# Kernel tuning notes

Hardware: AMD Instinct MI355X
Metric: run time of the kernel (lower is better)

Reference implementation:

```python
import jax, jax.numpy as jnp
import numpy as np

N, E, H, ATOM, BOND, G, DEPTH = 100000, 400000, 256, 133, 14, 512, 4


def _lin(k, out_dim, in_dim):
    kw, kb = jax.random.split(k)
    s = 1.0 / np.sqrt(in_dim)
    w = jax.random.uniform(kw, (out_dim, in_dim), jnp.float32, -s, s)
    b = jax.random.uniform(kb, (out_dim,), jnp.float32, -s, s)
    return w, b


def setup_inputs() -> dict:
    key = jax.random.key(0)
    ks = jax.random.split(key, 16)
    # paired directed edges: edge 2i and 2i+1 are reverses of each other
    src_half = jax.random.randint(ks[0], (E // 2,), 0, N)
    dst_half = jax.random.randint(ks[1], (E // 2,), 0, N)
    edge_src = jnp.stack([src_half, dst_half], axis=1).reshape(-1)
    edge_dst = jnp.stack([dst_half, src_half], axis=1).reshape(-1)
    b2rev = jnp.arange(E, dtype=jnp.int64) ^ 1
    node_to_graph = jnp.sort(jax.random.randint(ks[2], (N,), 0, G))
    atom_feats = jax.random.normal(ks[3], (N, ATOM), jnp.float32)
    edge_feats = jax.random.normal(ks[4], (E, BOND), jnp.float32)
    edge_weights = jax.random.uniform(ks[5], (E,), jnp.float32)
    Wi, _ = _lin(ks[6], H, ATOM + BOND)  # W_initial, bias=False
    Wm_w, Wm_b = _lin(ks[7], H, H)
    Wn_w, Wn_b = _lin(ks[8], H, ATOM + H)
    nh0_w, nh0_b = _lin(ks[9], H, H)
    nh2_w, nh2_b = _lin(ks[10], ATOM, H)
    eh0_w, eh0_b = _lin(ks[11], H, H)
    eh2_w, eh2_b = _lin(ks[12], BOND, H)
    gh0_w, gh0_b = _lin(ks[13], H, H)
    gh2_w, gh2_b = _lin(ks[14], 1, H)
    return dict(atom_feats=atom_feats, edge_feats=edge_feats, edge_weights=edge_weights,
                Wi=Wi, Wm_w=Wm_w, Wm_b=Wm_b, Wn_w=Wn_w, Wn_b=Wn_b,
                nh0_w=nh0_w, nh0_b=nh0_b, nh2_w=nh2_w, nh2_b=nh2_b,
                eh0_w=eh0_w, eh0_b=eh0_b, eh2_w=eh2_w, eh2_b=eh2_b,
                gh0_w=gh0_w, gh0_b=gh0_b, gh2_w=gh2_w, gh2_b=gh2_b,
                edge_src=edge_src, edge_dst=edge_dst, b2rev=b2rev,
                node_to_graph=node_to_graph, depth=DEPTH, num_graphs=G)


def reference(atom_feats, edge_feats, edge_weights, Wi, Wm_w, Wm_b, Wn_w, Wn_b,
              nh0_w, nh0_b, nh2_w, nh2_b, eh0_w, eh0_b, eh2_w, eh2_b,
              gh0_w, gh0_b, gh2_w, gh2_b,
              edge_src, edge_dst, b2rev, node_to_graph, depth, num_graphs):
    Nn = atom_feats.shape[0]
    valid = b2rev >= 0
    rev_idx = jnp.where(valid, b2rev, 0)
    # initial edge hidden states: [E, H]
    h = jax.nn.relu(jnp.concatenate([atom_feats[edge_src], edge_feats], axis=1) @ Wi.T)
    for _ in range(depth):
        # weighted scatter-add of edge messages onto destination nodes: [N, H]
        M = jax.ops.segment_sum(edge_weights[:, None] * h, edge_dst, num_segments=Nn)
        rev_h = jnp.where(valid[:, None], h[rev_idx], 0.0)
        rev_w = jnp.where(valid, edge_weights[rev_idx], 0.0)
        msg = M[edge_src] - rev_w[:, None] * rev_h  # [E, H]
        h = jax.nn.relu(msg @ Wm_w.T + Wm_b)
    node_agg = jax.ops.segment_sum(edge_weights[:, None] * h, edge_dst, num_segments=Nn)
    node_repr = jax.nn.relu(jnp.concatenate([atom_feats, node_agg], axis=1) @ Wn_w.T + Wn_b)
    graph_embeds = jax.ops.segment_sum(node_repr, node_to_graph, num_segments=num_graphs)
    pred_node = jax.nn.relu(node_repr @ nh0_w.T + nh0_b) @ nh2_w.T + nh2_b
    pred_edge = jax.nn.relu(h @ eh0_w.T + eh0_b) @ eh2_w.T + eh2_b
    pred_graph = (jax.nn.relu(graph_embeds @ gh0_w.T + gh0_b) @ gh2_w.T + gh2_b).squeeze(-1)
    return (pred_node, pred_edge, pred_graph, graph_embeds, node_repr, h)
```

## Files before the change

kernel.cpp:

```cpp
#include <hip/hip_runtime.h>
#include <hip/hip_bf16.h>

#define HDIM 256
#define ATOMF 133
#define BONDF 14
#define DEPTH_HC 4
#define SCAN_CHUNK 1024
#define KWN 448

typedef short bf16x8 __attribute__((ext_vector_type(8)));
typedef float f32x4 __attribute__((ext_vector_type(4)));
typedef unsigned short u16x8 __attribute__((ext_vector_type(8)));
typedef unsigned short u16x4 __attribute__((ext_vector_type(4)));

__device__ inline float bf2f(unsigned short u) {
    unsigned int x = ((unsigned int)u) << 16;
    float f; __builtin_memcpy(&f, &x, 4); return f;
}
__device__ inline unsigned short f2bf(float f) {
    __hip_bfloat16 h = __float2bfloat16(f);
    unsigned short u; __builtin_memcpy(&u, &h, 2); return u;
}

__device__ inline void gload_lds16(const unsigned short* g, unsigned short* lds) {
    __builtin_amdgcn_global_load_lds(
        (const __attribute__((address_space(1))) unsigned int*)g,
        (__attribute__((address_space(3))) unsigned int*)lds, 16, 0, 0);
}

__global__ __launch_bounds__(512) void mfma_gemm_cat(
    const float* __restrict__ atom, const float* __restrict__ bond,
    const int* __restrict__ src, int E,
    const unsigned short* __restrict__ W,
    unsigned short* __restrict__ Cb)
{
    __shared__ unsigned short As[128 * 32];
    __shared__ unsigned short Bs[256 * 32];
    const int t = threadIdx.x;
    const int w = t >> 6, l = t & 63;
    const int m0 = blockIdx.x * 128;
    const int wr = w >> 2, wc = w & 3;

    f32x4 acc[4][4] = {};

    const int ar = t >> 2;
    const int ac0 = (t & 3) * 8;
    long long e_row = m0 + ar; if (e_row > E - 1) e_row = E - 1;
    const int sn = src[e_row];
    const float* arow = atom + (size_t)sn * ATOMF;
    const float* brow = bond + (size_t)e_row * BONDF;

    const int kcol = (l & 3) * 8;
    const int rowL = (w << 4) + (l >> 2);

    #pragma unroll
    for (int k0 = 0; k0 < 160; k0 += 32) {
        u16x8 o;
        const int c = k0 + ac0;
        if (k0 < 128) {
            #pragma unroll
            for (int i = 0; i < 8; ++i) o[i] = f2bf(arow[c + i]);
        } else {
            #pragma unroll
            for (int i = 0; i < 8; ++i) {
                int k = c + i;
                float v = 0.0f;
                if (k < ATOMF)              v = arow[k];
                else if (k < ATOMF + BONDF) v = brow[k - ATOMF];
                o[i] = f2bf(v);
            }
        }
        *(u16x8*)&As[ar * 32 + ac0] = o;
        gload_lds16(W + (size_t)rowL * 160 + k0 + kcol, Bs + (size_t)w * 512);
        gload_lds16(W + (size_t)(128 + rowL) * 160 + k0 + kcol, Bs + 4096 + (size_t)w * 512);
        __syncthreads();

        const int kq = (l >> 4) * 8;
        const int rbase = (wr << 6) + (l & 15);
        const int cbase = (wc << 6) + (l & 15);
        bf16x8 af[4], bfr[4];
        #pragma unroll
        for (int i = 0; i < 4; ++i) {
            af[i]  = *(const bf16x8*)&As[(rbase + i * 16) * 32 + kq];
            bfr[i] = *(const bf16x8*)&Bs[(cbase + i * 16) * 32 + kq];
        }
        #pragma unroll
        for (int mi = 0; mi < 4; ++mi)
            #pragma unroll
            for (int ni = 0; ni < 4; ++ni)
                acc[mi][ni] = __builtin_amdgcn_mfma_f32_16x16x32_bf16(
                    af[mi], bfr[ni], acc[mi][ni], 0, 0, 0);
        __syncthreads();
    }

    const int ccol = l & 15, crow = (l >> 4) * 4;
    #pragma unroll
    for (int ni = 0; ni < 4; ++ni) {
        int gn = (wc << 6) + ni * 16 + ccol;
        #pragma unroll
        for (int mi = 0; mi < 4; ++mi) {
            #pragma unroll
            for (int j = 0; j < 4; ++j) {
                long long gm = m0 + (wr << 6) + mi * 16 + crow + j;
                if (gm >= E) continue;
                float v = fmaxf(acc[mi][ni][j], 0.0f);
                Cb[(size_t)gm * HDIM + gn] = f2bf(v);
            }
        }
    }
}

__global__ __launch_bounds__(512) void mfma_gemm_msg(
    const unsigned short* __restrict__ Mb,
    const unsigned short* __restrict__ h,
    const float* __restrict__ w,
    const int* __restrict__ src, int E,
    const unsigned short* __restrict__ W,
    const float* __restrict__ bias,
    float* __restrict__ Cf,
    unsigned short* __restrict__ Cb)
{
    __shared__ unsigned short As[128 * 32];
    __shared__ unsigned short Bs[256 * 32];
    const int t = threadIdx.x;
    const int wv = t >> 6, l = t & 63;
    const int m0 = blockIdx.x * 128;
    const int wr = wv >> 2, wc = wv & 3;

    f32x4 acc[4][4] = {};

    const int ar = t >> 2;
    const int ac0 = (t & 3) * 8;
    long long e_row = m0 + ar; if (e_row > E - 1) e_row = E - 1;
    const long long er1 = e_row ^ 1;
    const int sn = src[e_row];
    const float we1 = w[er1];

    const int kcol = (l & 3) * 8;
    const int rowL = (wv << 4) + (l >> 2);

    #pragma unroll
    for (int k0 = 0; k0 < 256; k0 += 32) {
        u16x8 Mv = *(const u16x8*)&Mb[(size_t)sn * HDIM + k0 + ac0];
        u16x8 hv = *(const u16x8*)&h[(size_t)er1 * HDIM + k0 + ac0];
        u16x8 o;
        #pragma unroll
        for (int i = 0; i < 8; ++i)
            o[i] = f2bf(bf2f(Mv[i]) - we1 * bf2f(hv[i]));
        *(u16x8*)&As[ar * 32 + ac0] = o;
        gload_lds16(W + (size_t)rowL * 256 + k0 + kcol, Bs + (size_t)wv * 512);
        gload_lds16(W + (size_t)(128 + rowL) * 256 + k0 + kcol, Bs + 4096 + (size_t)wv * 512);
        __syncthreads();

        const int kq = (l >> 4) * 8;
        const int rbase = (wr << 6) + (l & 15);
        const int cbase = (wc << 6) + (l & 15);
        bf16x8 af[4], bfr[4];
        #pragma unroll
        for (int i = 0; i < 4; ++i) {
            af[i]  = *(const bf16x8*)&As[(rbase + i * 16) * 32 + kq];
            bfr[i] = *(const bf16x8*)&Bs[(cbase + i * 16) * 32 + kq];
        }
        #pragma unroll
        for (int mi = 0; mi < 4; ++mi)
            #pragma unroll
            for (int ni = 0; ni < 4; ++ni)
                acc[mi][ni] = __builtin_amdgcn_mfma_f32_16x16x32_bf16(
                    af[mi], bfr[ni], acc[mi][ni], 0, 0, 0);
        __syncthreads();
    }

    const int ccol = l & 15, crow = (l >> 4) * 4;
    #pragma unroll
    for (int ni = 0; ni < 4; ++ni) {
        int gn = (wc << 6) + ni * 16 + ccol;
        float bv = bias[gn];
        #pragma unroll
        for (int mi = 0; mi < 4; ++mi) {
            #pragma unroll
            for (int j = 0; j < 4; ++j) {
                long long gm = m0 + (wr << 6) + mi * 16 + crow + j;
                if (gm >= E) continue;
                float v = fmaxf(acc[mi][ni][j] + bv, 0.0f);
                if (Cf) Cf[(size_t)gm * HDIM + gn] = v;
                Cb[(size_t)gm * HDIM + gn] = f2bf(v);
            }
        }
    }
}

__global__ __launch_bounds__(512) void mfma_gemm_catwn(
    const float* __restrict__ atom,
    const unsigned short* __restrict__ Mb,
    int N,
    const unsigned short* __restrict__ W,
    const float* __restrict__ bias,
    float* __restrict__ Cf,
    unsigned short* __restrict__ Cb)
{
    __shared__ unsigned short As[128 * 32];
    __shared__ unsigned short Bs[256 * 32];
    const int t = threadIdx.x;
    const int wv = t >> 6, l = t & 63;
    const int m0 = blockIdx.x * 128;
    const int wr = wv >> 2, wc = wv & 3;

    f32x4 acc[4][4] = {};

    const int ar = t >> 2;
    const int ac0 = (t & 3) * 8;
    long long nrow = m0 + ar; if (nrow > N - 1) nrow = N - 1;
    const float* arow = atom + (size_t)nrow * ATOMF;
    const unsigned short* mrow = Mb + (size_t)nrow * HDIM;

    const int kcol = (l & 3) * 8;
    const int rowL = (wv << 4) + (l >> 2);

    #pragma unroll
    for (int k0 = 0; k0 < KWN; k0 += 32) {
        const int c = k0 + ac0;
        u16x8 o;
        if (c + 8 <= ATOMF) {
            #pragma unroll
            for (int i = 0; i < 8; ++i) o[i] = f2bf(arow[c + i]);
        } else if (c >= 160 && c + 8 <= 416) {
            o = *(const u16x8*)&mrow[c - 160];
        } else if (c == 128) {
            #pragma unroll
            for (int i = 0; i < 8; ++i) o[i] = (c + i < ATOMF) ? f2bf(arow[c + i]) : (unsigned short)0;
        } else {
            #pragma unroll
            for (int i = 0; i < 8; ++i) o[i] = 0;
        }
        *(u16x8*)&As[ar * 32 + ac0] = o;
        gload_lds16(W + (size_t)rowL * KWN + k0 + kcol, Bs + (size_t)wv * 512);
        gload_lds16(W + (size_t)(128 + rowL) * KWN + k0 + kcol, Bs + 4096 + (size_t)wv * 512);
        __syncthreads();

        const int kq = (l >> 4) * 8;
        const int rbase = (wr << 6) + (l & 15);
        const int cbase = (wc << 6) + (l & 15);
        bf16x8 af[4], bfr[4];
        #pragma unroll
        for (int i = 0; i < 4; ++i) {
            af[i]  = *(const bf16x8*)&As[(rbase + i * 16) * 32 + kq];
            bfr[i] = *(const bf16x8*)&Bs[(cbase + i * 16) * 32 + kq];
        }
        #pragma unroll
        for (int mi = 0; mi < 4; ++mi)
            #pragma unroll
            for (int ni = 0; ni < 4; ++ni)
                acc[mi][ni] = __builtin_amdgcn_mfma_f32_16x16x32_bf16(
                    af[mi], bfr[ni], acc[mi][ni], 0, 0, 0);
        __syncthreads();
    }

    const int ccol = l & 15, crow = (l >> 4) * 4;
    #pragma unroll
    for (int ni = 0; ni < 4; ++ni) {
        int gn = (wc << 6) + ni * 16 + ccol;
        float bv = bias[gn];
        #pragma unroll
        for (int mi = 0; mi < 4; ++mi) {
            #pragma unroll
            for (int j = 0; j < 4; ++j) {
                long long gm = m0 + (wr << 6) + mi * 16 + crow + j;
                if (gm >= N) continue;
                float v = fmaxf(acc[mi][ni][j] + bv, 0.0f);
                Cf[(size_t)gm * HDIM + gn] = v;
                Cb[(size_t)gm * HDIM + gn] = f2bf(v);
            }
        }
    }
}

__global__ __launch_bounds__(512) void head_fused(
    const unsigned short* __restrict__ A, int Mrows,
    const unsigned short* __restrict__ W,
    const float* __restrict__ b0,
    const unsigned short* __restrict__ W2b,
    const float* __restrict__ b2,
    float* __restrict__ pred, int NOUT2)
{
    __shared__ unsigned short R[128 * 256];
    unsigned short* As = R;
    unsigned short* Bs = R + 128 * 32;
    const int t = threadIdx.x;
    const int w = t >> 6, l = t & 63;
    const int m0 = blockIdx.x * 128;
    const int wr = w >> 2, wc = w & 3;
    const int kq = (l >> 4) * 8;

    f32x4 acc[4][4] = {};
    const int kcol = (l & 3) * 8;
    const int rowL = (w << 4) + (l >> 2);

    #pragma unroll
    for (int k0 = 0; k0 < 256; k0 += 32) {
        long long r0 = m0 + rowL; if (r0 > Mrows - 1) r0 = Mrows - 1;
        gload_lds16(A + (size_t)r0 * 256 + k0 + kcol, As + (size_t)w * 512);
        gload_lds16(W + (size_t)rowL * 256 + k0 + kcol, Bs + (size_t)w * 512);
        gload_lds16(W + (size_t)(128 + rowL) * 256 + k0 + kcol, Bs + 4096 + (size_t)w * 512);
        __syncthreads();

        const int rbase = (wr << 6) + (l & 15);
        const int cbase = (wc << 6) + (l & 15);
        bf16x8 af[4], bfr[4];
        #pragma unroll
        for (int i = 0; i < 4; ++i) {
            af[i]  = *(const bf16x8*)&As[(rbase + i * 16) * 32 + kq];
            bfr[i] = *(const bf16x8*)&Bs[(cbase + i * 16) * 32 + kq];
        }
        #pragma unroll
        for (int mi = 0; mi < 4; ++mi)
            #pragma unroll
            for (int ni = 0; ni < 4; ++ni)
                acc[mi][ni] = __builtin_amdgcn_mfma_f32_16x16x32_bf16(
                    af[mi], bfr[ni], acc[mi][ni], 0, 0, 0);
        __syncthreads();
    }

    const int ccol = l & 15, crow = (l >> 4) * 4;
    #pragma unroll
    for (int ni = 0; ni < 4; ++ni) {
        const int col = (wc << 6) + ni * 16 + ccol;
        const float bv = b0[col];
        #pragma unroll
        for (int mi = 0; mi < 4; ++mi) {
            #pragma unroll
            for (int j = 0; j < 4; ++j) {
                const int rr = (wr << 6) + mi * 16 + crow + j;
                float v = fmaxf(acc[mi][ni][j] + bv, 0.0f);
                size_t byteoff = ((size_t)rr * 512 + (size_t)col * 2) ^ (size_t)((rr & 7) << 4);
                *(unsigned short*)((char*)R + byteoff) = f2bf(v);
            }
        }
    }
    __syncthreads();

    const int erow = (w << 4) + (l & 15);
    const int jrow = l & 15;
    for (int cc = 0; cc * 16 < NOUT2; ++cc) {
        bf16x8 w2b[8];
        #pragma unroll
        for (int ks = 0; ks < 8; ++ks)
            w2b[ks] = *(const bf16x8*)&W2b[(size_t)(cc * 16 + jrow) * 256 + ks * 32 + kq];
        f32x4 acc2 = {};
        #pragma unroll
        for (int ks = 0; ks < 8; ++ks) {
            size_t byteoff = ((size_t)erow * 512 + (size_t)(ks * 64 + kq * 2))
                             ^ (size_t)((erow & 7) << 4);
            bf16x8 af;
            __builtin_memcpy(&af, (char*)R + byteoff, 16);
            acc2 = __builtin_amdgcn_mfma_f32_16x16x32_bf16(af, w2b[ks], acc2, 0, 0, 0);
        }
        const int col = cc * 16 + jrow;
        if (col < NOUT2) {
            #pragma unroll
            for (int j = 0; j < 4; ++j) {
                long long gm = m0 + (w << 4) + (l >> 4) * 4 + j;
                if (gm < Mrows) pred[gm * NOUT2 + col] = acc2[j] + b2[col];
            }
        }
    }
}

__global__ void pad_all(const float* Wi, const float* Wm, const float* Wn,
                        const float* n0, const float* n2, const float* e0, const float* e2,
                        unsigned short* Wib, unsigned short* Wmb, unsigned short* Wnb,
                        unsigned short* n0b, unsigned short* n2b, unsigned short* e0b,
                        unsigned short* e2b) {
    int wid = blockIdx.x >> 8;
    int r = blockIdx.x & 255;
    if (wid == 2) {
        for (int c = threadIdx.x; c < KWN; c += blockDim.x) {
            float v = 0.0f;
            if (c < ATOMF)                 v = Wn[(size_t)r * 389 + c];
            else if (c >= 160 && c < 416)  v = Wn[(size_t)r * 389 + (c - 160 + ATOMF)];
            Wnb[(size_t)r * KWN + c] = f2bf(v);
        }
        return;
    }
    const float* S; unsigned short* D; int R, C, Cp;
    switch (wid) {
        case 0: S = Wi; D = Wib; R = 256; C = 147; Cp = 160; break;
        case 1: S = Wm; D = Wmb; R = 256; C = 256; Cp = 256; break;
        case 3: S = n0; D = n0b; R = 256; C = 256; Cp = 256; break;
        case 4: S = n2; D = n2b; R = 133; C = 256; Cp = 256; break;
        case 5: S = e0; D = e0b; R = 256; C = 256; Cp = 256; break;
        default: S = e2; D = e2b; R = 14;  C = 256; Cp = 256; break;
    }
    for (int c = threadIdx.x; c < Cp; c += blockDim.x) {
        float v = (r < R && c < C) ? S[(size_t)r * C + c] : 0.0f;
        D[(size_t)r * Cp + c] = f2bf(v);
    }
}

__global__ void count_dst(const int* __restrict__ dst, int* __restrict__ cnt, int E) {
    int e = blockIdx.x * 256 + threadIdx.x;
    if (e < E) atomicAdd(&cnt[dst[e]], 1);
}

__global__ void scan_reduce(const int* __restrict__ cnt, int* __restrict__ csum, int n) {
    __shared__ int s[256];
    int base = blockIdx.x * SCAN_CHUNK;
    int v = 0;
    for (int i = threadIdx.x; i < SCAN_CHUNK; i += 256) {
        int idx = base + i;
        v += (idx < n) ? cnt[idx] : 0;
    }
    s[threadIdx.x] = v; __syncthreads();
    for (int o = 128; o > 0; o >>= 1) {
        if (threadIdx.x < o) s[threadIdx.x] += s[threadIdx.x + o];
        __syncthreads();
    }
    if (threadIdx.x == 0) csum[blockIdx.x] = s[0];
}

__global__ void scan_sums(const int* __restrict__ csum, int* __restrict__ coff, int nchunks) {
    __shared__ int s[1024];
    int t = threadIdx.x;
    s[t] = (t < nchunks) ? csum[t] : 0;
    __syncthreads();
    for (int o = 1; o < 1024; o <<= 1) {
        int v = (t >= o) ? s[t - o] : 0;
        __syncthreads();
        s[t] += v;
        __syncthreads();
    }
    if (t < nchunks) coff[t] = (t == 0) ? 0 : s[t - 1];
}

__global__ void scan_apply(const int* __restrict__ cnt, const int* __restrict__ coff,
                           int* __restrict__ off, int* __restrict__ cursor, int n) {
    __shared__ int s[256];
    int b = blockIdx.x, t = threadIdx.x;
    int base = b * SCAN_CHUNK + t * 4;
    int v[4];
    #pragma unroll
    for (int i = 0; i < 4; ++i) v[i] = (base + i < n) ? cnt[base + i] : 0;
    s[t] = v[0] + v[1] + v[2] + v[3];
    __syncthreads();
    for (int o = 1; o < 256; o <<= 1) {
        int x = (t >= o) ? s[t - o] : 0;
        __syncthreads();
        s[t] += x;
        __syncthreads();
    }
    int run = coff[b] + ((t > 0) ? s[t - 1] : 0);
    #pragma unroll
    for (int i = 0; i < 4; ++i) {
        if (base + i < n) cursor[base + i] = run;
        run += v[i];
        if (base + i < n) off[base + i + 1] = run;
    }
}

__global__ void fill_elist(const int* __restrict__ dst, int* __restrict__ cursor,
                           int* __restrict__ elist, int E) {
    int e = blockIdx.x * 256 + threadIdx.x;
    if (e < E) {
        int p = atomicAdd(&cursor[dst[e]], 1);
        elist[p] = e;
    }
}

__global__ void sort_buckets(const int* __restrict__ off, int* __restrict__ elist, int N) {
    int n = blockIdx.x * 256 + threadIdx.x;
    if (n >= N) return;
    int s = off[n], t = off[n + 1];
    for (int i = s; i < t - 1; ++i) {
        int mn = elist[i], mi = i;
        for (int j = i + 1; j < t; ++j) {
            int v = elist[j];
            if (v < mn) { mn = v; mi = j; }
        }
        if (mi != i) { elist[mi] = elist[i]; elist[i] = mn; }
    }
}

__global__ void gather_M(const unsigned short* __restrict__ h, const float* __restrict__ w,
                         const int* __restrict__ off, const int* __restrict__ elist,
                         unsigned short* __restrict__ Mb, int N) {
    int n = blockIdx.x * 4 + (threadIdx.x >> 6);
    if (n >= N) return;
    int c = (threadIdx.x & 63) * 4;
    int s = off[n], e_ = off[n + 1];
    float4 acc = {0.f, 0.f, 0.f, 0.f};
    for (int i = s; i < e_; i += 4) {
        int m = e_ - i;
        int f[4]; float wf[4]; u16x4 hv[4];
        #pragma unroll
        for (int j = 0; j < 4; ++j) if (j < m) f[j] = elist[i + j];
        #pragma unroll
        for (int j = 0; j < 4; ++j) if (j < m) {
            wf[j] = w[f[j]];
            hv[j] = *(const u16x4*)&h[(size_t)f[j] * HDIM + c];
        }
        #pragma unroll
        for (int j = 0; j < 4; ++j) if (j < m) {
            acc.x += wf[j] * bf2f(hv[j][0]);
            acc.y += wf[j] * bf2f(hv[j][1]);
            acc.z += wf[j] * bf2f(hv[j][2]);
            acc.w += wf[j] * bf2f(hv[j][3]);
        }
    }
    u16x4 o;
    o[0] = f2bf(acc.x); o[1] = f2bf(acc.y); o[2] = f2bf(acc.z); o[3] = f2bf(acc.w);
    *(u16x4*)&Mb[(size_t)n * HDIM + c] = o;
}

__global__ void graph_sum(const float* __restrict__ nr, const int* __restrict__ n2g,
                          float* __restrict__ ge, int N) {
    int g = blockIdx.x, t = threadIdx.x;
    int lo = 0, hi = N;
    while (lo < hi) { int mid = (lo + hi) >> 1; if (n2g[mid] < g) lo = mid + 1; else hi = mid; }
    int start = lo;
    hi = N;
    while (lo < hi) { int mid = (lo + hi) >> 1; if (n2g[mid] < g + 1) lo = mid + 1; else hi = mid; }
    int end = lo;
    float acc = 0.0f;
    for (int n = start; n < end; ++n) acc += nr[(size_t)n * HDIM + t];
    ge[(size_t)g * HDIM + t] = acc;
}

__global__ __launch_bounds__(256) void gemm_f32(const float* __restrict__ A, int lda,
                                                const float* __restrict__ W,
                                                const float* __restrict__ bias,
                                                float* __restrict__ C, int ldc,
                                                int Mrows, int Nout, int K, int relu) {
    __shared__ float Asm[16][64];
    __shared__ float Bsm[16][64];
    int t = threadIdx.x;
    int m0 = blockIdx.x * 64, n0 = blockIdx.y * 64;
    int tx = t & 15, ty = t >> 4, ml = t >> 2, kk = (t & 3) * 4;
    float acc[4][4] = {};
    for (int k0 = 0; k0 < K; k0 += 16) {
        #pragma unroll
        for (int i = 0; i < 4; ++i) {
            int k = k0 + kk + i, m = m0 + ml, n = n0 + ml;
            Asm[kk + i][ml] = (m < Mrows && k < K) ? A[(size_t)m * lda + k] : 0.0f;
            Bsm[kk + i][ml] = (n < Nout  && k < K) ? W[(size_t)n * K + k]  : 0.0f;
        }
        __syncthreads();
        #pragma unroll
        for (int k = 0; k < 16; ++k) {
            float4 av = *(const float4*)&Asm[k][ty << 2];
            float4 bv = *(const float4*)&Bsm[k][tx << 2];
            float a4[4] = {av.x, av.y, av.z, av.w};
            float b4[4] = {bv.x, bv.y, bv.z, bv.w};
            #pragma unroll
            for (int i = 0; i < 4; ++i)
                #pragma unroll
                for (int j = 0; j < 4; ++j)
                    acc[i][j] = fmaf(a4[i], b4[j], acc[i][j]);
        }
        __syncthreads();
    }
    #pragma unroll
    for (int i = 0; i < 4; ++i) {
        int m = m0 + (ty << 2) + i;
        if (m >= Mrows) continue;
        #pragma unroll
        for (int j = 0; j < 4; ++j) {
            int n = n0 + (tx << 2) + j;
            if (n >= Nout) continue;
            float v = acc[i][j];
            if (bias) v += bias[n];
            if (relu) v = fmaxf(v, 0.0f);
            C[(size_t)m * ldc + n] = v;
        }
    }
}

extern "C" void kernel_launch(void* const* d_in, const int* in_sizes, int n_in,
                              void* d_out, int out_size, void* d_ws, size_t ws_size,
                              hipStream_t stream) {
    const float* atom_feats   = (const float*)d_in[0];
    const float* edge_feats   = (const float*)d_in[1];
    const float* edge_weights = (const float*)d_in[2];
    const float* Wi    = (const float*)d_in[3];
    const float* Wm_w  = (const float*)d_in[4];
    const float* Wm_b  = (const float*)d_in[5];
    const float* Wn_w  = (const float*)d_in[6];
    const float* Wn_b  = (const float*)d_in[7];
    const float* nh0_w = (const float*)d_in[8];
    const float* nh0_b = (const float*)d_in[9];
    const float* nh2_w = (const float*)d_in[10];
    const float* nh2_b = (const float*)d_in[11];
    const float* eh0_w = (const float*)d_in[12];
    const float* eh0_b = (const float*)d_in[13];
    const float* eh2_w = (const float*)d_in[14];
    const float* eh2_b = (const float*)d_in[15];
    const float* gh0_w = (const float*)d_in[16];
    const float* gh0_b = (const float*)d_in[17];
    const float* gh2_w = (const float*)d_in[18];
    const float* gh2_b = (const float*)d_in[19];
    const int* edge_src      = (const int*)d_in[20];
    const int* edge_dst      = (const int*)d_in[21];
    const int* node_to_graph = (const int*)d_in[23];

    int N = in_sizes[0] / ATOMF;
    int E = in_sizes[1] / BONDF;
    long long G = ((long long)out_size - (long long)N * (ATOMF + HDIM)
                   - (long long)E * (BONDF + HDIM)) / (1 + HDIM);

    float* out = (float*)d_out;
    float* pred_node = out;
    float* pred_edge = pred_node + (size_t)N * ATOMF;
    float* pred_grph = pred_edge + (size_t)E * BONDF;
    float* gemb      = pred_grph + (size_t)G;
    float* node_repr = gemb + (size_t)G * HDIM;
    float* h_f32     = node_repr + (size_t)N * HDIM;

    unsigned short* hA  = (unsigned short*)d_ws;
    unsigned short* hB  = hA + (size_t)E * HDIM;
    unsigned short* Mb  = hB + (size_t)E * HDIM;
    unsigned short* Wib  = Mb + (size_t)N * HDIM;
    unsigned short* Wmb  = Wib + 256 * 160;
    unsigned short* Wnb  = Wmb + 256 * 256;
    unsigned short* nh0b = Wnb + 256 * KWN;
    unsigned short* nh2b = nh0b + 256 * 256;
    unsigned short* eh0b = nh2b + 256 * 256;
    unsigned short* eh2b = eh0b + 256 * 256;
    int* csr = (int*)(eh2b + 256 * 256);
    int* cnt    = csr;
    int* off    = cnt + N;
    int* cursor = off + N + 1;
    int* elist  = cursor + N;
    int* csum   = elist + E;
    int* coff   = csum + 1024;
    float* gtmp = (float*)(coff + 1024);

    int nchunks = (N + SCAN_CHUNK - 1) / SCAN_CHUNK;

    hipMemsetAsync(cnt, 0, (size_t)N * sizeof(int), stream);
    count_dst<<<(E + 255) / 256, 256, 0, stream>>>(edge_dst, cnt, E);
    scan_reduce<<<nchunks, 256, 0, stream>>>(cnt, csum, N);
    scan_sums<<<1, 1024, 0, stream>>>(csum, coff, nchunks);
    hipMemsetAsync(off, 0, sizeof(int), stream);
    scan_apply<<<nchunks, 256, 0, stream>>>(cnt, coff, off, cursor, N);
    fill_elist<<<(E + 255) / 256, 256, 0, stream>>>(edge_dst, cursor, elist, E);
    sort_buckets<<<(N + 255) / 256, 256, 0, stream>>>(off, elist, N);

    pad_all<<<7 * 256, 256, 0, stream>>>(Wi, Wm_w, Wn_w, nh0_w, nh2_w, eh0_w, eh2_w,
                                         Wib, Wmb, Wnb, nh0b, nh2b, eh0b, eh2b);

    mfma_gemm_cat<<<(E + 127) / 128, 512, 0, stream>>>(atom_feats, edge_feats, edge_src,
                                                       E, Wib, hA);

    int ngrid = (N + 3) / 4;
    unsigned short* hc = hA;
    unsigned short* hn = hB;
    for (int d = 0; d < DEPTH_HC; ++d) {
        gather_M<<<ngrid, 256, 0, stream>>>(hc, edge_weights, off, elist, Mb, N);
        float* cf = (d == DEPTH_HC - 1) ? h_f32 : nullptr;
        mfma_gemm_msg<<<(E + 127) / 128, 512, 0, stream>>>(
            Mb, hc, edge_weights, edge_src, E, Wmb, Wm_b, cf, hn);
        unsigned short* tmp = hc; hc = hn; hn = tmp;
    }

    head_fused<<<(E + 127) / 128, 512, 0, stream>>>(hc, E, eh0b, eh0_b, eh2b, eh2_b,
                                                    pred_edge, BONDF);

    gather_M<<<ngrid, 256, 0, stream>>>(hc, edge_weights, off, elist, Mb, N);
    mfma_gemm_catwn<<<(N + 127) / 128, 512, 0, stream>>>(atom_feats, Mb, N, Wnb, Wn_b,
                                                         node_repr, hB);

    graph_sum<<<(int)G, HDIM, 0, stream>>>(node_repr, node_to_graph, gemb, N);

    head_fused<<<(N + 127) / 128, 512, 0, stream>>>(hB, N, nh0b, nh0_b, nh2b, nh2_b,
                                                    pred_node, ATOMF);

    dim3 g0((G + 63) / 64, 4);
    gemm_f32<<<g0, 256, 0, stream>>>(gemb, HDIM, gh0_w, gh0_b, gtmp, HDIM, (int)G, HDIM, HDIM, 1);
    dim3 g1((G + 63) / 64, 1);
    gemm_f32<<<g1, 256, 0, stream>>>(gtmp, HDIM, gh2_w, gh2_b, pred_grph, 1, (int)G, 1, HDIM, 0);
}
```

Before: 2.076 ms.

## Pre-convert atoms to padded bf16, prefetch GEMM A-tiles, fuse graph head

Converts atom features once into a padded bf16 buffer so the edge and node GEMMs load 16-byte vectors instead of converting scattered fp32 values. The A-operand loads in the cat, message and node GEMMs are software-prefetched one k-step ahead, overlapping the gathers with MFMA work. The Wn K dimension shrinks from 448 to 416 by dropping padding. The two fp32 graph-head GEMMs become one fused per-graph kernel, and a memset moves into scan_apply. These changes add an extra conversion kernel and more live registers.

```diff
diff --git a/kernel.cpp b/kernel.cpp
--- a/kernel.cpp
+++ b/kernel.cpp
@@ -6,7 +6,7 @@
 #define BONDF 14
 #define DEPTH_HC 4
 #define SCAN_CHUNK 1024
-#define KWN 448
+#define KWN 416
 
 typedef short bf16x8 __attribute__((ext_vector_type(8)));
 typedef float f32x4 __attribute__((ext_vector_type(4)));
@@ -29,7 +29,8 @@
 }
 
 __global__ __launch_bounds__(512) void mfma_gemm_cat(
-    const float* __restrict__ atom, const float* __restrict__ bond,
+    const unsigned short* __restrict__ atomb,
+    const float* __restrict__ bond,
     const int* __restrict__ src, int E,
     const unsigned short* __restrict__ W,
     unsigned short* __restrict__ Cb)
@@ -47,29 +48,25 @@
     const int ac0 = (t & 3) * 8;
     long long e_row = m0 + ar; if (e_row > E - 1) e_row = E - 1;
     const int sn = src[e_row];
-    const float* arow = atom + (size_t)sn * ATOMF;
+    const unsigned short* arow = atomb + (size_t)sn * 160;
     const float* brow = bond + (size_t)e_row * BONDF;
+
+    u16x8 tail = *(const u16x8*)&arow[128 + ac0];
+    #pragma unroll
+    for (int i = 0; i < 8; ++i) {
+        int k = 128 + ac0 + i;
+        if (k >= ATOMF && k < ATOMF + BONDF) tail[i] = f2bf(brow[k - ATOMF]);
+    }
+    u16x8 cur = *(const u16x8*)&arow[ac0];
 
     const int kcol = (l & 3) * 8;
     const int rowL = (w << 4) + (l >> 2);
 
     #pragma unroll
     for (int k0 = 0; k0 < 160; k0 += 32) {
-        u16x8 o;
-        const int c = k0 + ac0;
-        if (k0 < 128) {
-            #pragma unroll
-            for (int i = 0; i < 8; ++i) o[i] = f2bf(arow[c + i]);
-        } else {
-            #pragma unroll
-            for (int i = 0; i < 8; ++i) {
-                int k = c + i;
-                float v = 0.0f;
-                if (k < ATOMF)              v = arow[k];
-                else if (k < ATOMF + BONDF) v = brow[k - ATOMF];
-                o[i] = f2bf(v);
-            }
-        }
+        u16x8 nxt = cur;
+        if (k0 + 32 < 128) nxt = *(const u16x8*)&arow[k0 + 32 + ac0];
+        u16x8 o = (k0 == 128) ? tail : cur;
         *(u16x8*)&As[ar * 32 + ac0] = o;
         gload_lds16(W + (size_t)rowL * 160 + k0 + kcol, Bs + (size_t)w * 512);
         gload_lds16(W + (size_t)(128 + rowL) * 160 + k0 + kcol, Bs + 4096 + (size_t)w * 512);
@@ -91,6 +88,7 @@
                 acc[mi][ni] = __builtin_amdgcn_mfma_f32_16x16x32_bf16(
                     af[mi], bfr[ni], acc[mi][ni], 0, 0, 0);
         __syncthreads();
+        cur = nxt;
     }
 
     const int ccol = l & 15, crow = (l >> 4) * 4;
@@ -135,14 +133,22 @@
     const long long er1 = e_row ^ 1;
     const int sn = src[e_row];
     const float we1 = w[er1];
+    const unsigned short* mrow = Mb + (size_t)sn * HDIM;
+    const unsigned short* hrow = h + (size_t)er1 * HDIM;
+
+    u16x8 Mv = *(const u16x8*)&mrow[ac0];
+    u16x8 hv = *(const u16x8*)&hrow[ac0];
 
     const int kcol = (l & 3) * 8;
     const int rowL = (wv << 4) + (l >> 2);
 
     #pragma unroll
     for (int k0 = 0; k0 < 256; k0 += 32) {
-        u16x8 Mv = *(const u16x8*)&Mb[(size_t)sn * HDIM + k0 + ac0];
-        u16x8 hv = *(const u16x8*)&h[(size_t)er1 * HDIM + k0 + ac0];
+        u16x8 Mn = Mv, hn2 = hv;
+        if (k0 + 32 < 256) {
+            Mn  = *(const u16x8*)&mrow[k0 + 32 + ac0];
+            hn2 = *(const u16x8*)&hrow[k0 + 32 + ac0];
+        }
         u16x8 o;
         #pragma unroll
         for (int i = 0; i < 8; ++i)
@@ -168,6 +174,7 @@
                 acc[mi][ni] = __builtin_amdgcn_mfma_f32_16x16x32_bf16(
                     af[mi], bfr[ni], acc[mi][ni], 0, 0, 0);
         __syncthreads();
+        Mv = Mn; hv = hn2;
     }
 
     const int ccol = l & 15, crow = (l >> 4) * 4;
@@ -190,7 +197,7 @@
 }
 
 __global__ __launch_bounds__(512) void mfma_gemm_catwn(
-    const float* __restrict__ atom,
+    const unsigned short* __restrict__ atomb,
     const unsigned short* __restrict__ Mb,
     int N,
     const unsigned short* __restrict__ W,
@@ -210,29 +217,22 @@
     const int ar = t >> 2;
     const int ac0 = (t & 3) * 8;
     long long nrow = m0 + ar; if (nrow > N - 1) nrow = N - 1;
-    const float* arow = atom + (size_t)nrow * ATOMF;
+    const unsigned short* arow = atomb + (size_t)nrow * 160;
     const unsigned short* mrow = Mb + (size_t)nrow * HDIM;
+
+    u16x8 cur = *(const u16x8*)&arow[ac0];
 
     const int kcol = (l & 3) * 8;
     const int rowL = (wv << 4) + (l >> 2);
 
     #pragma unroll
     for (int k0 = 0; k0 < KWN; k0 += 32) {
-        const int c = k0 + ac0;
-        u16x8 o;
-        if (c + 8 <= ATOMF) {
-            #pragma unroll
-            for (int i = 0; i < 8; ++i) o[i] = f2bf(arow[c + i]);
-        } else if (c >= 160 && c + 8 <= 416) {
-            o = *(const u16x8*)&mrow[c - 160];
-        } else if (c == 128) {
-            #pragma unroll
-            for (int i = 0; i < 8; ++i) o[i] = (c + i < ATOMF) ? f2bf(arow[c + i]) : (unsigned short)0;
-        } else {
-            #pragma unroll
-            for (int i = 0; i < 8; ++i) o[i] = 0;
-        }
-        *(u16x8*)&As[ar * 32 + ac0] = o;
+        u16x8 nxt = cur;
+        if (k0 + 32 <= 128)
+            nxt = *(const u16x8*)&arow[k0 + 32 + ac0];
+        else if (k0 + 32 >= 160 && k0 + 32 <= 384)
+            nxt = *(const u16x8*)&mrow[k0 + 32 - 160 + ac0];
+        *(u16x8*)&As[ar * 32 + ac0] = cur;
         gload_lds16(W + (size_t)rowL * KWN + k0 + kcol, Bs + (size_t)wv * 512);
         gload_lds16(W + (size_t)(128 + rowL) * KWN + k0 + kcol, Bs + 4096 + (size_t)wv * 512);
         __syncthreads();
@@ -253,6 +253,7 @@
                 acc[mi][ni] = __builtin_amdgcn_mfma_f32_16x16x32_bf16(
                     af[mi], bfr[ni], acc[mi][ni], 0, 0, 0);
         __syncthreads();
+        cur = nxt;
     }
 
     const int ccol = l & 15, crow = (l >> 4) * 4;
@@ -365,6 +366,14 @@
     }
 }
 
+__global__ __launch_bounds__(640) void atom_conv(const float* __restrict__ a,
+                                                 unsigned short* __restrict__ ab, int N) {
+    int n = blockIdx.x * 4 + threadIdx.x / 160;
+    int c = threadIdx.x % 160;
+    if (n >= N) return;
+    ab[(size_t)n * 160 + c] = (c < ATOMF) ? f2bf(a[(size_t)n * ATOMF + c]) : (unsigned short)0;
+}
+
 __global__ void pad_all(const float* Wi, const float* Wm, const float* Wn,
                         const float* n0, const float* n2, const float* e0, const float* e2,
                         unsigned short* Wib, unsigned short* Wmb, unsigned short* Wnb,
@@ -375,8 +384,8 @@
     if (wid == 2) {
         for (int c = threadIdx.x; c < KWN; c += blockDim.x) {
             float v = 0.0f;
-            if (c < ATOMF)                 v = Wn[(size_t)r * 389 + c];
-            else if (c >= 160 && c < 416)  v = Wn[(size_t)r * 389 + (c - 160 + ATOMF)];
+            if (c < ATOMF)      v = Wn[(size_t)r * 389 + c];
+            else if (c >= 160)  v = Wn[(size_t)r * 389 + (c - 27)];
             Wnb[(size_t)r * KWN + c] = f2bf(v);
         }
         return;
@@ -435,6 +444,7 @@
                            int* __restrict__ off, int* __restrict__ cursor, int n) {
     __shared__ int s[256];
     int b = blockIdx.x, t = threadIdx.x;
+    if (b == 0 && t == 0) off[0] = 0;
     int base = b * SCAN_CHUNK + t * 4;
     int v[4];
     #pragma unroll
@@ -524,53 +534,30 @@
     ge[(size_t)g * HDIM + t] = acc;
 }
 
-__global__ __launch_bounds__(256) void gemm_f32(const float* __restrict__ A, int lda,
-                                                const float* __restrict__ W,
-                                                const float* __restrict__ bias,
-                                                float* __restrict__ C, int ldc,
-                                                int Mrows, int Nout, int K, int relu) {
-    __shared__ float Asm[16][64];
-    __shared__ float Bsm[16][64];
+__global__ __launch_bounds__(256) void graph_head(
+    const float* __restrict__ ge,
+    const float* __restrict__ w0, const float* __restrict__ b0,
+    const float* __restrict__ w2, const float* __restrict__ b2,
+    float* __restrict__ pred, int G)
+{
+    int g = blockIdx.x;
+    if (g >= G) return;
+    __shared__ float xs[256];
+    __shared__ float ys[256];
     int t = threadIdx.x;
-    int m0 = blockIdx.x * 64, n0 = blockIdx.y * 64;
-    int tx = t & 15, ty = t >> 4, ml = t >> 2, kk = (t & 3) * 4;
-    float acc[4][4] = {};
-    for (int k0 = 0; k0 < K; k0 += 16) {
-        #pragma unroll
-        for (int i = 0; i < 4; ++i) {
-            int k = k0 + kk + i, m = m0 + ml, n = n0 + ml;
-            Asm[kk + i][ml] = (m < Mrows && k < K) ? A[(size_t)m * lda + k] : 0.0f;
-            Bsm[kk + i][ml] = (n < Nout  && k < K) ? W[(size_t)n * K + k]  : 0.0f;
-        }
-        __syncthreads();
-        #pragma unroll
-        for (int k = 0; k < 16; ++k) {
-            float4 av = *(const float4*)&Asm[k][ty << 2];
-            float4 bv = *(const float4*)&Bsm[k][tx << 2];
-            float a4[4] = {av.x, av.y, av.z, av.w};
-            float b4[4] = {bv.x, bv.y, bv.z, bv.w};
-            #pragma unroll
-            for (int i = 0; i < 4; ++i)
-                #pragma unroll
-                for (int j = 0; j < 4; ++j)
-                    acc[i][j] = fmaf(a4[i], b4[j], acc[i][j]);
-        }
-        __syncthreads();
-    }
-    #pragma unroll
-    for (int i = 0; i < 4; ++i) {
-        int m = m0 + (ty << 2) + i;
-        if (m >= Mrows) continue;
-        #pragma unroll
-        for (int j = 0; j < 4; ++j) {
-            int n = n0 + (tx << 2) + j;
-            if (n >= Nout) continue;
-            float v = acc[i][j];
-            if (bias) v += bias[n];
-            if (relu) v = fmaxf(v, 0.0f);
-            C[(size_t)m * ldc + n] = v;
-        }
-    }
+    xs[t] = ge[(size_t)g * 256 + t];
+    __syncthreads();
+    float acc = b0[t];
+    const float* wr = w0 + (size_t)t * 256;
+    #pragma unroll 8
+    for (int k = 0; k < 256; ++k) acc = fmaf(wr[k], xs[k], acc);
+    ys[t] = fmaxf(acc, 0.0f) * w2[t];
+    __syncthreads();
+    for (int o = 128; o > 0; o >>= 1) {
+        if (t < o) ys[t] += ys[t + o];
+        __syncthreads();
+    }
+    if (t == 0) pred[g] = ys[0] + b2[0];
 }
 
 extern "C" void kernel_launch(void* const* d_in, const int* in_sizes, int n_in,
@@ -613,16 +600,17 @@
     float* node_repr = gemb + (size_t)G * HDIM;
     float* h_f32     = node_repr + (size_t)N * HDIM;
 
-    unsigned short* hA  = (unsigned short*)d_ws;
-    unsigned short* hB  = hA + (size_t)E * HDIM;
-    unsigned short* Mb  = hB + (size_t)E * HDIM;
-    unsigned short* Wib  = Mb + (size_t)N * HDIM;
-    unsigned short* Wmb  = Wib + 256 * 160;
-    unsigned short* Wnb  = Wmb + 256 * 256;
-    unsigned short* nh0b = Wnb + 256 * KWN;
-    unsigned short* nh2b = nh0b + 256 * 256;
-    unsigned short* eh0b = nh2b + 256 * 256;
-    unsigned short* eh2b = eh0b + 256 * 256;
+    unsigned short* hA    = (unsigned short*)d_ws;
+    unsigned short* hB    = hA + (size_t)E * HDIM;
+    unsigned short* Mb    = hB + (size_t)E * HDIM;
+    unsigned short* atomb = Mb + (size_t)N * HDIM;
+    unsigned short* Wib   = atomb + (size_t)N * 160;
+    unsigned short* Wmb   = Wib + 256 * 160;
+    unsigned short* Wnb   = Wmb + 256 * 256;
+    unsigned short* nh0b  = Wnb + 256 * KWN;
+    unsigned short* nh2b  = nh0b + 256 * 256;
+    unsigned short* eh0b  = nh2b + 256 * 256;
+    unsigned short* eh2b  = eh0b + 256 * 256;
     int* csr = (int*)(eh2b + 256 * 256);
     int* cnt    = csr;
     int* off    = cnt + N;
@@ -630,7 +618,6 @@
     int* elist  = cursor + N;
     int* csum   = elist + E;
     int* coff   = csum + 1024;
-    float* gtmp = (float*)(coff + 1024);
 
     int nchunks = (N + SCAN_CHUNK - 1) / SCAN_CHUNK;
 
@@ -638,15 +625,15 @@
     count_dst<<<(E + 255) / 256, 256, 0, stream>>>(edge_dst, cnt, E);
     scan_reduce<<<nchunks, 256, 0, stream>>>(cnt, csum, N);
     scan_sums<<<1, 1024, 0, stream>>>(csum, coff, nchunks);
-    hipMemsetAsync(off, 0, sizeof(int), stream);
     scan_apply<<<nchunks, 256, 0, stream>>>(cnt, coff, off, cursor, N);
     fill_elist<<<(E + 255) / 256, 256, 0, stream>>>(edge_dst, cursor, elist, E);
     sort_buckets<<<(N + 255) / 256, 256, 0, stream>>>(off, elist, N);
 
     pad_all<<<7 * 256, 256, 0, stream>>>(Wi, Wm_w, Wn_w, nh0_w, nh2_w, eh0_w, eh2_w,
                                          Wib, Wmb, Wnb, nh0b, nh2b, eh0b, eh2b);
-
-    mfma_gemm_cat<<<(E + 127) / 128, 512, 0, stream>>>(atom_feats, edge_feats, edge_src,
+    atom_conv<<<(N + 3) / 4, 640, 0, stream>>>(atom_feats, atomb, N);
+
+    mfma_gemm_cat<<<(E + 127) / 128, 512, 0, stream>>>(atomb, edge_feats, edge_src,
                                                        E, Wib, hA);
 
     int ngrid = (N + 3) / 4;
@@ -664,7 +651,7 @@
                                                     pred_edge, BONDF);
 
     gather_M<<<ngrid, 256, 0, stream>>>(hc, edge_weights, off, elist, Mb, N);
-    mfma_gemm_catwn<<<(N + 127) / 128, 512, 0, stream>>>(atom_feats, Mb, N, Wnb, Wn_b,
+    mfma_gemm_catwn<<<(N + 127) / 128, 512, 0, stream>>>(atomb, Mb, N, Wnb, Wn_b,
                                                          node_repr, hB);
 
     graph_sum<<<(int)G, HDIM, 0, stream>>>(node_repr, node_to_graph, gemb, N);
@@ -672,8 +659,6 @@
     head_fused<<<(N + 127) / 128, 512, 0, stream>>>(hB, N, nh0b, nh0_b, nh2b, nh2_b,
                                                     pred_node, ATOMF);
 
-    dim3 g0((G + 63) / 64, 4);
-    gemm_f32<<<g0, 256, 0, stream>>>(gemb, HDIM, gh0_w, gh0_b, gtmp, HDIM, (int)G, HDIM, HDIM, 1);
-    dim3 g1((G + 63) / 64, 1);
-    gemm_f32<<<g1, 256, 0, stream>>>(gtmp, HDIM, gh2_w, gh2_b, pred_grph, 1, (int)G, 1, HDIM, 0);
-}
+    graph_head<<<(int)G, 256, 0, stream>>>(gemb, gh0_w, gh0_b, gh2_w, gh2_b,
+                                           pred_grph, (int)G);
+}
```

Result: no change. 2.049 ms (-1.3%).
